# Optimization experiments

Measured on AMD Instinct MI355X. Metric: run time of the kernel, lower is better.

The kernel has to match this reference:

```python
import jax, jax.numpy as jnp
import numpy as np

N = 50000
E = 1600000
IN = 128
HID = 128
OUT = 64
NL = 200000
NEG_SLOPE = 0.2


def _glorot(key, shape):
    fan_in, fan_out = shape[0], shape[-1]
    s = jnp.sqrt(6.0 / (fan_in + fan_out))
    return jax.random.uniform(key, shape, jnp.float32, -s, s)


def setup_inputs() -> dict:
    key = jax.random.key(0)
    ks = jax.random.split(key, 16)
    x = jax.random.normal(ks[0], (N, IN), jnp.float32)
    edge_index = jax.random.randint(ks[1], (2, E), 0, N, dtype=jnp.int32)
    edge_label_index = jax.random.randint(ks[2], (2, NL), 0, N, dtype=jnp.int32)
    return {
        "x": x,
        "edge_index": edge_index,
        "edge_label_index": edge_label_index,
        "W1": _glorot(ks[3], (IN, HID)),  "a1s": _glorot(ks[4], (HID,)),  "a1d": _glorot(ks[5], (HID,)),  "b1": jnp.zeros((HID,), jnp.float32),
        "W2": _glorot(ks[6], (HID, HID)), "a2s": _glorot(ks[7], (HID,)),  "a2d": _glorot(ks[8], (HID,)),  "b2": jnp.zeros((HID,), jnp.float32),
        "W3": _glorot(ks[9], (HID, HID)), "a3s": _glorot(ks[10], (HID,)), "a3d": _glorot(ks[11], (HID,)), "b3": jnp.zeros((HID,), jnp.float32),
        "W4": _glorot(ks[12], (HID, OUT)), "b4": jnp.zeros((OUT,), jnp.float32),
    }


def _add_self_loops(edge_index, n):
    loop = jnp.arange(n, dtype=edge_index.dtype)
    return jnp.concatenate([edge_index, jnp.stack([loop, loop])], axis=1)


def gat_conv(x, edge_index, W, a_s, a_d, b):
    """PyG GATConv, heads=1, add_self_loops=True: gather, LeakyReLU score,
    segment softmax over destination nodes, scatter-add aggregate."""
    n = x.shape[0]
    ei = _add_self_loops(edge_index, n)
    src, dst = ei[0], ei[1]
    h = x @ W                                    # [N, H]
    e = jax.nn.leaky_relu((h @ a_s)[src] + (h @ a_d)[dst], NEG_SLOPE)  # [E']
    m = jax.ops.segment_max(e, dst, num_segments=n)
    p = jnp.exp(e - m[dst])
    s = jax.ops.segment_sum(p, dst, num_segments=n)
    alpha = p / s[dst]                           # segment softmax
    out = jax.ops.segment_sum(h[src] * alpha[:, None], dst, num_segments=n)
    return out + b


def gcn_conv(x, edge_index, W, b):
    """PyG GCNConv: self-loops + symmetric degree normalization."""
    n = x.shape[0]
    ei = _add_self_loops(edge_index, n)
    src, dst = ei[0], ei[1]
    h = x @ W
    deg = jax.ops.segment_sum(jnp.ones(src.shape, h.dtype), dst, num_segments=n)
    dinv = jax.lax.rsqrt(deg)
    norm = dinv[src] * dinv[dst]                 # [E']
    out = jax.ops.segment_sum(h[src] * norm[:, None], dst, num_segments=n)
    return out + b


def reference(x, edge_index, edge_label_index,
              W1, a1s, a1d, b1, W2, a2s, a2d, b2,
              W3, a3s, a3d, b3, W4, b4):
    h = jax.nn.relu(gat_conv(x, edge_index, W1, a1s, a1d, b1))
    h = jax.nn.relu(gat_conv(h, edge_index, W2, a2s, a2d, b2))
    h = jax.nn.relu(gat_conv(h, edge_index, W3, a3s, a3d, b3))
    z = gcn_conv(h, edge_index, W4, b4)          # [N, OUT]
    # decode: dot product of endpoint embeddings -> link logits [NL]
    return (z[edge_label_index[0]] * z[edge_label_index[1]]).sum(axis=-1)
```

## Files before the change

### kernel.cpp

```cpp
#include <hip/hip_runtime.h>
#include <hip/hip_fp16.h>
#include <math.h>

#define NN   50000
#define NE   1600000
#define DHID 128
#define DOUTC 64
#define NLBL 200000
#define CAP  80
#define NEG  0.2f
#define NBK  196
#define CAPB 8800
#define CHK  4096

typedef unsigned short u16;
typedef _Float16 half8 __attribute__((ext_vector_type(8)));
typedef float floatx4 __attribute__((ext_vector_type(4)));
typedef unsigned int u32x4 __attribute__((ext_vector_type(4)));


__global__ __launch_bounds__(256) void k_bin(const int* __restrict__ ei,
                                             int* __restrict__ gcnt,
                                             unsigned* __restrict__ bins) {
    __shared__ int cntL[NBK];
    __shared__ int offL[NBK];
    __shared__ int curL[NBK];
    __shared__ int curG[NBK];
    __shared__ unsigned stage[CHK];
    const int tid = threadIdx.x;
    const int e0 = blockIdx.x * CHK + tid * 16;
    const bool act = (e0 + 15) < NE;

    unsigned pk[16];
    int bb[16];
    if (act) {
#pragma unroll
        for (int g = 0; g < 4; ++g) {
            int4 s4 = *(const int4*)&ei[e0 + g * 4];
            int4 d4 = *(const int4*)&ei[NE + e0 + g * 4];
            int sa[4] = {s4.x, s4.y, s4.z, s4.w};
            int da[4] = {d4.x, d4.y, d4.z, d4.w};
#pragma unroll
            for (int k = 0; k < 4; ++k) {
                int idx = g * 4 + k;
                bb[idx] = da[k] >> 8;
                pk[idx] = (unsigned)sa[k] | ((unsigned)(da[k] & 255) << 16)
                        | ((unsigned)bb[idx] << 24);
            }
        }
    }
    for (int i = tid; i < NBK; i += 256) cntL[i] = 0;
    __syncthreads();
    if (act) {
#pragma unroll
        for (int k = 0; k < 16; ++k) atomicAdd(&cntL[bb[k]], 1);
    }
    __syncthreads();
    if (tid < NBK) {
        int acc = 0;
        for (int i = 0; i < tid; ++i) acc += cntL[i];
        offL[tid] = acc;
        curL[tid] = acc;
    }
    __syncthreads();
    for (int i = tid; i < NBK; i += 256) curG[i] = atomicAdd(&gcnt[i], cntL[i]);
    __syncthreads();
    if (act) {
#pragma unroll
        for (int k = 0; k < 16; ++k) {
            int pos = atomicAdd(&curL[bb[k]], 1);
            stage[pos] = pk[k];
        }
    }
    __syncthreads();
    const int tot = offL[NBK - 1] + cntL[NBK - 1];
    for (int j = tid; j < tot; j += 256) {
        unsigned v = stage[j];
        int b = v >> 24;
        int lr = j - offL[b];
        bins[(size_t)b * CAPB + curG[b] + lr] = v & 0x00FFFFFFu;
    }
}

__global__ __launch_bounds__(256) void k_build(const unsigned* __restrict__ bins,
                                               const int* __restrict__ gcnt,
                                               int* __restrict__ cnt,
                                               u16* __restrict__ csr) {
    __shared__ u16 rows[256 * CAP];
    __shared__ int cur[256];
    const int b = blockIdx.x, tid = threadIdx.x;
    const int d0 = b << 8;
    const int nd = min(256, NN - d0);
    if (tid < nd) { cur[tid] = 1; rows[tid * CAP] = (u16)(d0 + tid); }
    __syncthreads();
    const int n = gcnt[b];
    for (int i = tid; i < n; i += 256) {
        unsigned v = bins[(size_t)b * CAPB + i];
        int s = v & 0xFFFF, dl = (v >> 16) & 0xFF;
        int pos = atomicAdd(&cur[dl], 1);
        if (pos < CAP) rows[dl * CAP + pos] = (u16)s;
    }
    __syncthreads();
    const unsigned* rw = (const unsigned*)rows;
    unsigned* cw = (unsigned*)(csr + (size_t)d0 * CAP);
    const int tot = nd * (CAP / 2);
    for (int i = tid; i < tot; i += 256) cw[i] = rw[i];
    if (tid < nd) cnt[d0 + tid] = cur[tid];
}


__global__ __launch_bounds__(256) void k_prep_w(const float* __restrict__ W1f,
                                                const float* __restrict__ W2f,
                                                const float* __restrict__ W3f,
                                                const float* __restrict__ W4f,
                                                half8* __restrict__ Wf1,
                                                half8* __restrict__ Wf2,
                                                half8* __restrict__ Wf3,
                                                half8* __restrict__ Wf4,
                                                int* __restrict__ gcnt) {
    if (blockIdx.x == 28) {
        int i = threadIdx.x;
        if (i < NBK) gcnt[i] = 0;
        return;
    }
    int e = blockIdx.x * 256 + threadIdx.x;
    const float* W;
    half8* Wf;
    int nout, le;
    if (e < 2048)      { W = W1f; Wf = Wf1; nout = 128; le = e; }
    else if (e < 4096) { W = W2f; Wf = Wf2; nout = 128; le = e - 2048; }
    else if (e < 6144) { W = W3f; Wf = Wf3; nout = 128; le = e - 4096; }
    else               { W = W4f; Wf = Wf4; nout = 64;  le = e - 6144; }
    int c = le >> 8, rem = le & 255, ks = rem >> 6, lane = rem & 63;
    int n = lane & 15, quad = lane >> 4;
    int col = c * 16 + n, k0 = ks * 32 + quad * 8;
    half8 v;
#pragma unroll
    for (int j = 0; j < 8; ++j) v[j] = (_Float16)W[(size_t)(k0 + j) * nout + col];
    Wf[le] = v;
}


template <int NOUT, bool ATTN, typename TA>
__global__ __launch_bounds__(256) void gemm_mfma(const TA* __restrict__ A0,
                                                 const TA* __restrict__ A1,
                                                 const half8* __restrict__ Wf,
                                                 __half* __restrict__ C0,
                                                 __half* __restrict__ C1,
                                                 const float* __restrict__ a_s,
                                                 const float* __restrict__ a_d,
                                                 float* __restrict__ asv,
                                                 float* __restrict__ adv, int M) {
    constexpr int CT = NOUT / 16;
    const int tid = threadIdx.x;
    const int wave = tid >> 6, lane = tid & 63;
    const int n = lane & 15, quad = lane >> 4;
    const int row0 = blockIdx.x * 64 + wave * 16;

    const int row = row0 + n;
    const bool ok = row < M;
    half8 a[4];
    half8 zz = {};
#pragma unroll
    for (int ks = 0; ks < 4; ++ks) {
        if (!ok) { a[ks] = zz; continue; }
        int c128 = ks * 32 + quad * 8;
        if constexpr (sizeof(TA) == 2) {
            const TA* Ah = (c128 < 64) ? A0 : A1;
            a[ks] = *(const half8*)((const _Float16*)Ah + (size_t)row * 64 + (c128 & 63));
        } else {
            const float* Ap = (const float*)A0 + (size_t)row * 128 + c128;
            float4 f0 = *(const float4*)Ap;
            float4 f1 = *(const float4*)(Ap + 4);
            half8 v;
            v[0] = (_Float16)f0.x; v[1] = (_Float16)f0.y; v[2] = (_Float16)f0.z; v[3] = (_Float16)f0.w;
            v[4] = (_Float16)f1.x; v[5] = (_Float16)f1.y; v[6] = (_Float16)f1.z; v[7] = (_Float16)f1.w;
            a[ks] = v;
        }
    }

    floatx4 acc[CT];
#pragma unroll
    for (int c = 0; c < CT; ++c) acc[c] = (floatx4){0.f, 0.f, 0.f, 0.f};

#pragma unroll
    for (int c = 0; c < CT; ++c) {
#pragma unroll
        for (int ks = 0; ks < 4; ++ks) {
            half8 b = Wf[(c * 4 + ks) * 64 + lane];
            acc[c] = __builtin_amdgcn_mfma_f32_16x16x32_f16(b, a[ks], acc[c], 0, 0, 0);
        }
    }

    if (ok) {
#pragma unroll
        for (int c = 0; c < CT; ++c) {
            __half* Ch = (NOUT == 64 || c < 4) ? C0 : C1;
            int coff = (NOUT == 64 || c < 4) ? c * 16 : (c - 4) * 16;
            __half2 h0 = __floats2half2_rn(acc[c][0], acc[c][1]);
            __half2 h1 = __floats2half2_rn(acc[c][2], acc[c][3]);
            uint2 u;
            __builtin_memcpy(&u.x, &h0, 4);
            __builtin_memcpy(&u.y, &h1, 4);
            *(uint2*)&Ch[(size_t)row * 64 + coff + quad * 4] = u;
        }
    }

    if (ATTN) {
        float ps = 0.f, pd = 0.f;
#pragma unroll
        for (int c = 0; c < CT; ++c) {
#pragma unroll
            for (int reg = 0; reg < 4; ++reg) {
                float w = acc[c][reg];
                ps = fmaf(w, a_s[c * 16 + quad * 4 + reg], ps);
                pd = fmaf(w, a_d[c * 16 + quad * 4 + reg], pd);
            }
        }
        ps += __shfl_xor(ps, 16); ps += __shfl_xor(ps, 32);
        pd += __shfl_xor(pd, 16); pd += __shfl_xor(pd, 32);
        if (quad == 0 && ok) { asv[row] = ps; adv[row] = pd; }
    }
}

__device__ inline void fma_h8v(half8 h, float al, float* acc) {
#pragma unroll
    for (int k = 0; k < 8; ++k) acc[k] = fmaf(al, (float)h[k], acc[k]);
}


__global__ __launch_bounds__(256) void k_gat_agg(const __half* __restrict__ h0,
                                                 const __half* __restrict__ h1,
                                                 const int* __restrict__ cnt,
                                                 const u16* __restrict__ csr,
                                                 const float* __restrict__ asv,
                                                 const float* __restrict__ adv,
                                                 const float* __restrict__ bias,
                                                 __half* __restrict__ out0,
                                                 __half* __restrict__ out1) {
    __shared__ float alsL[4][88];
    __shared__ int   srcL[4][88];
    int lane = threadIdx.x & 63, wv = threadIdx.x >> 6;
    int d = blockIdx.x * 4 + wv;
    if (d >= NN) return;
    int deg = cnt[d]; if (deg > CAP) deg = CAP;
    const float advd = adv[d];
    const u16* rowp = csr + (size_t)d * CAP;

    int j0 = lane, j1 = lane + 64;
    int s0 = 0, s1 = 0;
    float e0 = -INFINITY, e1 = -INFINITY;
    if (j0 < deg) {
        s0 = rowp[j0];
        float t = asv[s0] + advd;
        e0 = (t >= 0.f) ? t : NEG * t;
    }
    if (j1 < deg) {
        s1 = rowp[j1];
        float t = asv[s1] + advd;
        e1 = (t >= 0.f) ? t : NEG * t;
    }
    float m = fmaxf(e0, e1);
#pragma unroll
    for (int off = 32; off; off >>= 1) m = fmaxf(m, __shfl_xor(m, off));
    float p0 = (j0 < deg) ? __expf(e0 - m) : 0.f;
    float p1 = (j1 < deg) ? __expf(e1 - m) : 0.f;
    float s = p0 + p1;
#pragma unroll
    for (int off = 32; off; off >>= 1) s += __shfl_xor(s, off);
    float inv = 1.f / s;
    alsL[wv][j0] = p0 * inv;
    srcL[wv][j0] = s0;
    if (j1 < 88) { alsL[wv][j1] = p1 * inv; srcL[wv][j1] = s1; }

    int slot = lane >> 3, r = lane & 7;
    int degp = (deg + 7) & ~7;
#pragma unroll
    for (int half = 0; half < 2; ++half) {
        const __half* ht = half ? h1 : h0;
        __half* ot = half ? out1 : out0;
        float acc[8];
#pragma unroll
        for (int k = 0; k < 8; ++k) acc[k] = 0.f;

        for (int base = 0; base < degp; base += 8) {
            int idx = base + slot;
            float al = alsL[wv][idx];
            int   sj = srcL[wv][idx];
            half8 hv = *(const half8*)&ht[(size_t)sj * 64 + r * 8];
            fma_h8v(hv, al, acc);
        }
#pragma unroll
        for (int k = 0; k < 8; ++k) {
            acc[k] += __shfl_xor(acc[k], 8);
            acc[k] += __shfl_xor(acc[k], 16);
            acc[k] += __shfl_xor(acc[k], 32);
        }
        if (slot == 0) {
            __half2 ho[4];
#pragma unroll
            for (int k = 0; k < 4; ++k) {
                float oa = fmaxf(acc[2 * k]     + bias[half * 64 + r * 8 + 2 * k],     0.f);
                float ob = fmaxf(acc[2 * k + 1] + bias[half * 64 + r * 8 + 2 * k + 1], 0.f);
                ho[k] = __floats2half2_rn(oa, ob);
            }
            u32x4 u;
            __builtin_memcpy(&u, &ho[0], 16);
            __builtin_nontemporal_store(u, (u32x4*)&ot[(size_t)d * 64 + r * 8]);
        }
    }
}


__global__ __launch_bounds__(256) void k_gcn_agg(const __half* __restrict__ h,
                                                 const int* __restrict__ cnt,
                                                 const u16* __restrict__ csr,
                                                 const float* __restrict__ bias,
                                                 __half* __restrict__ z) {
    __shared__ float nmL[4][88];
    __shared__ int   srcL[4][88];
    int lane = threadIdx.x & 63, wv = threadIdx.x >> 6;
    int d = blockIdx.x * 4 + wv;
    if (d >= NN) return;
    int degc = cnt[d];
    int deg = degc > CAP ? CAP : degc;
    float did = rsqrtf((float)degc);
    const u16* rowp = csr + (size_t)d * CAP;

    int j0 = lane, j1 = lane + 64;
    int s0 = 0, s1 = 0;
    float n0 = 0.f, n1 = 0.f;
    if (j0 < deg) { s0 = rowp[j0]; n0 = rsqrtf((float)cnt[s0]) * did; }
    if (j1 < deg) { s1 = rowp[j1]; n1 = rsqrtf((float)cnt[s1]) * did; }
    nmL[wv][j0] = n0;
    srcL[wv][j0] = s0;
    if (j1 < 88) { nmL[wv][j1] = n1; srcL[wv][j1] = s1; }

    int slot = lane >> 3, r = lane & 7;
    float acc[8];
#pragma unroll
    for (int k = 0; k < 8; ++k) acc[k] = 0.f;

    int degp = (deg + 7) & ~7;
    for (int base = 0; base < degp; base += 8) {
        int idx = base + slot;
        float nm = nmL[wv][idx];
        int   sj = srcL[wv][idx];
        half8 hv = *(const half8*)&h[(size_t)sj * 64 + r * 8];
        fma_h8v(hv, nm, acc);
    }
#pragma unroll
    for (int k = 0; k < 8; ++k) {
        acc[k] += __shfl_xor(acc[k], 8);
        acc[k] += __shfl_xor(acc[k], 16);
        acc[k] += __shfl_xor(acc[k], 32);
    }
    if (slot == 0) {
        __half2 ho[4];
#pragma unroll
        for (int k = 0; k < 4; ++k) {
            float oa = acc[2 * k]     + bias[r * 8 + 2 * k];
            float ob = acc[2 * k + 1] + bias[r * 8 + 2 * k + 1];
            ho[k] = __floats2half2_rn(oa, ob);
        }
        uint4 u;
        __builtin_memcpy(&u, &ho[0], 16);
        *(uint4*)&z[(size_t)d * 64 + r * 8] = u;
    }
}


__global__ __launch_bounds__(256) void k_decode(const __half* __restrict__ z,
                                                const int* __restrict__ eli,
                                                float* __restrict__ outp) {
    int lane = threadIdx.x & 63, wv = threadIdx.x >> 6;
    int g = lane >> 4, r = lane & 15;
    int idx = (blockIdx.x * 4 + wv) * 4 + g;
    if (idx >= NLBL) return;
    int a = eli[idx], b = eli[NLBL + idx];
    uint2 ua = *(const uint2*)&z[(size_t)a * 64 + r * 4];
    uint2 ub = *(const uint2*)&z[(size_t)b * 64 + r * 4];
    float2 a0 = __half22float2(*(__half2*)&ua.x);
    float2 a1 = __half22float2(*(__half2*)&ua.y);
    float2 b0 = __half22float2(*(__half2*)&ub.x);
    float2 b1 = __half22float2(*(__half2*)&ub.y);
    float v = a0.x * b0.x + a0.y * b0.y + a1.x * b1.x + a1.y * b1.y;
#pragma unroll
    for (int off = 8; off; off >>= 1) v += __shfl_xor(v, off);
    if (r == 0) outp[idx] = v;
}


extern "C" void kernel_launch(void* const* d_in, const int* in_sizes, int n_in,
                              void* d_out, int out_size, void* d_ws, size_t ws_size,
                              hipStream_t stream) {
    const float* x   = (const float*)d_in[0];
    const int*   ei  = (const int*)d_in[1];
    const int*   eli = (const int*)d_in[2];
    const float* W1 = (const float*)d_in[3];
    const float* a1s = (const float*)d_in[4];
    const float* a1d = (const float*)d_in[5];
    const float* b1 = (const float*)d_in[6];
    const float* W2 = (const float*)d_in[7];
    const float* a2s = (const float*)d_in[8];
    const float* a2d = (const float*)d_in[9];
    const float* b2 = (const float*)d_in[10];
    const float* W3 = (const float*)d_in[11];
    const float* a3s = (const float*)d_in[12];
    const float* a3d = (const float*)d_in[13];
    const float* b3 = (const float*)d_in[14];
    const float* W4 = (const float*)d_in[15];
    const float* b4 = (const float*)d_in[16];
    float* outp = (float*)d_out;

    char* p = (char*)d_ws;
    auto alloc = [&](size_t bytes) -> char* {
        char* r = p;
        p += (bytes + 255) & ~(size_t)255;
        return r;
    };
    int*    cnt  = (int*)alloc((size_t)NN * 4);
    u16*    csr  = (u16*)alloc((size_t)NN * CAP * 2);
    int*    gcnt = (int*)alloc((size_t)NBK * 4);
    float*  asv  = (float*)alloc((size_t)NN * 4);
    float*  advv = (float*)alloc((size_t)NN * 4);
    __half* G0   = (__half*)alloc((size_t)NN * 64 * 2);
    __half* G1   = (__half*)alloc((size_t)NN * 64 * 2);
    __half* B1a  = (__half*)alloc((size_t)NN * 64 * 2);
    __half* B1b  = (__half*)alloc((size_t)NN * 64 * 2);
    __half* B2a  = (__half*)alloc((size_t)NN * 64 * 2);
    __half* B2b  = (__half*)alloc((size_t)NN * 64 * 2);
    __half* zf   = (__half*)alloc((size_t)NN * 64 * 2);
    half8*  Wf1  = (half8*)alloc(2048 * 16);
    half8*  Wf2  = (half8*)alloc(2048 * 16);
    half8*  Wf3  = (half8*)alloc(2048 * 16);
    half8*  Wf4  = (half8*)alloc(1024 * 16);
    unsigned* bins = (unsigned*)alloc((size_t)NBK * CAPB * 4);

    const int gBin  = (NE + CHK - 1) / CHK;
    const int gGemm = (NN + 63) / 64;
    const int gNode = (NN + 3) / 4;
    const int gDec  = (NLBL + 15) / 16;

    k_prep_w<<<29, 256, 0, stream>>>(W1, W2, W3, W4, Wf1, Wf2, Wf3, Wf4, gcnt);
    k_bin<<<gBin, 256, 0, stream>>>(ei, gcnt, bins);
    k_build<<<NBK, 256, 0, stream>>>(bins, gcnt, cnt, csr);

    gemm_mfma<128, true, float><<<gGemm, 256, 0, stream>>>(x, x, Wf1, G0, G1, a1s, a1d, asv, advv, NN);
    k_gat_agg<<<gNode, 256, 0, stream>>>(G0, G1, cnt, csr, asv, advv, b1, B1a, B1b);

    gemm_mfma<128, true, __half><<<gGemm, 256, 0, stream>>>(B1a, B1b, Wf2, G0, G1, a2s, a2d, asv, advv, NN);
    k_gat_agg<<<gNode, 256, 0, stream>>>(G0, G1, cnt, csr, asv, advv, b2, B2a, B2b);

    gemm_mfma<128, true, __half><<<gGemm, 256, 0, stream>>>(B2a, B2b, Wf3, G0, G1, a3s, a3d, asv, advv, NN);
    k_gat_agg<<<gNode, 256, 0, stream>>>(G0, G1, cnt, csr, asv, advv, b3, B1a, B1b);

    gemm_mfma<64, false, __half><<<gGemm, 256, 0, stream>>>(B1a, B1b, Wf4, G0, G0, nullptr, nullptr, nullptr, nullptr, NN);
    k_gcn_agg<<<gNode, 256, 0, stream>>>(G0, cnt, csr, b4, zf);

    k_decode<<<gDec, 256, 0, stream>>>(zf, eli, outp);
}
```

Before: 383.9 us.

## Fuse edge binning with first-layer GEMM and use single-wave GEMM blocks

Merges the edge-binning kernel and the layer-1 projection GEMM into one launch, with block index choosing the role, so the independent GEMM work can run alongside binning and one launch is saved. The later GEMMs are launched as 64-thread blocks, one 16-row tile each, instead of 256-thread blocks. Bounds checks are simplified because NN is a multiple of 16. The shared-memory footprint of the binning phase now applies to the GEMM blocks too, which may limit occupancy.

```diff
diff --git a/kernel.cpp b/kernel.cpp
--- a/kernel.cpp
+++ b/kernel.cpp
@@ -4,14 +4,13 @@
 
 #define NN   50000
 #define NE   1600000
-#define DHID 128
-#define DOUTC 64
 #define NLBL 200000
 #define CAP  80
 #define NEG  0.2f
 #define NBK  196
 #define CAPB 8800
 #define CHK  4096
+#define GBIN 391
 
 typedef unsigned short u16;
 typedef _Float16 half8 __attribute__((ext_vector_type(8)));
@@ -19,16 +18,15 @@
 typedef unsigned int u32x4 __attribute__((ext_vector_type(4)));
 
 
-__global__ __launch_bounds__(256) void k_bin(const int* __restrict__ ei,
-                                             int* __restrict__ gcnt,
-                                             unsigned* __restrict__ bins) {
+__device__ void ph_bin(int blk, const int* __restrict__ ei,
+                       int* __restrict__ gcnt, unsigned* __restrict__ bins) {
     __shared__ int cntL[NBK];
     __shared__ int offL[NBK];
     __shared__ int curL[NBK];
     __shared__ int curG[NBK];
     __shared__ unsigned stage[CHK];
     const int tid = threadIdx.x;
-    const int e0 = blockIdx.x * CHK + tid * 16;
+    const int e0 = blk * CHK + tid * 16;
     const bool act = (e0 + 15) < NE;
 
     unsigned pk[16];
@@ -109,15 +107,15 @@
 }
 
 
-__global__ __launch_bounds__(256) void k_prep_w(const float* __restrict__ W1f,
-                                                const float* __restrict__ W2f,
-                                                const float* __restrict__ W3f,
-                                                const float* __restrict__ W4f,
-                                                half8* __restrict__ Wf1,
-                                                half8* __restrict__ Wf2,
-                                                half8* __restrict__ Wf3,
-                                                half8* __restrict__ Wf4,
-                                                int* __restrict__ gcnt) {
+__global__ __launch_bounds__(256) void k_pre(const float* __restrict__ W1f,
+                                             const float* __restrict__ W2f,
+                                             const float* __restrict__ W3f,
+                                             const float* __restrict__ W4f,
+                                             half8* __restrict__ Wf1,
+                                             half8* __restrict__ Wf2,
+                                             half8* __restrict__ Wf3,
+                                             half8* __restrict__ Wf4,
+                                             int* __restrict__ gcnt) {
     if (blockIdx.x == 28) {
         int i = threadIdx.x;
         if (i < NBK) gcnt[i] = 0;
@@ -142,28 +140,24 @@
 
 
 template <int NOUT, bool ATTN, typename TA>
-__global__ __launch_bounds__(256) void gemm_mfma(const TA* __restrict__ A0,
-                                                 const TA* __restrict__ A1,
-                                                 const half8* __restrict__ Wf,
-                                                 __half* __restrict__ C0,
-                                                 __half* __restrict__ C1,
-                                                 const float* __restrict__ a_s,
-                                                 const float* __restrict__ a_d,
-                                                 float* __restrict__ asv,
-                                                 float* __restrict__ adv, int M) {
+__device__ __forceinline__ void gemm_tile(int gt, int lane,
+                                          const TA* __restrict__ A0,
+                                          const TA* __restrict__ A1,
+                                          const half8* __restrict__ Wf,
+                                          __half* __restrict__ C0,
+                                          __half* __restrict__ C1,
+                                          const float* __restrict__ a_s,
+                                          const float* __restrict__ a_d,
+                                          float* __restrict__ asv,
+                                          float* __restrict__ adv) {
     constexpr int CT = NOUT / 16;
-    const int tid = threadIdx.x;
-    const int wave = tid >> 6, lane = tid & 63;
     const int n = lane & 15, quad = lane >> 4;
-    const int row0 = blockIdx.x * 64 + wave * 16;
-
-    const int row = row0 + n;
-    const bool ok = row < M;
+    if (gt * 16 >= NN) return;
+    const int row = gt * 16 + n;
+
     half8 a[4];
-    half8 zz = {};
 #pragma unroll
     for (int ks = 0; ks < 4; ++ks) {
-        if (!ok) { a[ks] = zz; continue; }
         int c128 = ks * 32 + quad * 8;
         if constexpr (sizeof(TA) == 2) {
             const TA* Ah = (c128 < 64) ? A0 : A1;
@@ -182,7 +176,6 @@
     floatx4 acc[CT];
 #pragma unroll
     for (int c = 0; c < CT; ++c) acc[c] = (floatx4){0.f, 0.f, 0.f, 0.f};
-
 #pragma unroll
     for (int c = 0; c < CT; ++c) {
 #pragma unroll
@@ -192,18 +185,16 @@
         }
     }
 
-    if (ok) {
-#pragma unroll
-        for (int c = 0; c < CT; ++c) {
-            __half* Ch = (NOUT == 64 || c < 4) ? C0 : C1;
-            int coff = (NOUT == 64 || c < 4) ? c * 16 : (c - 4) * 16;
-            __half2 h0 = __floats2half2_rn(acc[c][0], acc[c][1]);
-            __half2 h1 = __floats2half2_rn(acc[c][2], acc[c][3]);
-            uint2 u;
-            __builtin_memcpy(&u.x, &h0, 4);
-            __builtin_memcpy(&u.y, &h1, 4);
-            *(uint2*)&Ch[(size_t)row * 64 + coff + quad * 4] = u;
-        }
+#pragma unroll
+    for (int c = 0; c < CT; ++c) {
+        __half* Ch = (NOUT == 64 || c < 4) ? C0 : C1;
+        int coff = (NOUT == 64 || c < 4) ? c * 16 : (c - 4) * 16;
+        __half2 h0 = __floats2half2_rn(acc[c][0], acc[c][1]);
+        __half2 h1 = __floats2half2_rn(acc[c][2], acc[c][3]);
+        uint2 u;
+        __builtin_memcpy(&u.x, &h0, 4);
+        __builtin_memcpy(&u.y, &h1, 4);
+        *(uint2*)&Ch[(size_t)row * 64 + coff + quad * 4] = u;
     }
 
     if (ATTN) {
@@ -219,11 +210,41 @@
         }
         ps += __shfl_xor(ps, 16); ps += __shfl_xor(ps, 32);
         pd += __shfl_xor(pd, 16); pd += __shfl_xor(pd, 32);
-        if (quad == 0 && ok) { asv[row] = ps; adv[row] = pd; }
-    }
-}
-
-__device__ inline void fma_h8v(half8 h, float al, float* acc) {
+        if (quad == 0) { asv[row] = ps; adv[row] = pd; }
+    }
+}
+
+__global__ __launch_bounds__(256) void k_bin_gemm1(const int* __restrict__ ei,
+                                                   int* __restrict__ gcnt,
+                                                   unsigned* __restrict__ bins,
+                                                   const float* __restrict__ x,
+                                                   const half8* __restrict__ Wf1,
+                                                   __half* __restrict__ G0,
+                                                   __half* __restrict__ G1,
+                                                   const float* __restrict__ a_s,
+                                                   const float* __restrict__ a_d,
+                                                   float* __restrict__ asv,
+                                                   float* __restrict__ adv) {
+    if (blockIdx.x < GBIN) { ph_bin(blockIdx.x, ei, gcnt, bins); return; }
+    int gt = (blockIdx.x - GBIN) * 4 + (threadIdx.x >> 6);
+    gemm_tile<128, true, float>(gt, threadIdx.x & 63, x, x, Wf1, G0, G1, a_s, a_d, asv, adv);
+}
+
+template <int NOUT, bool ATTN>
+__global__ __launch_bounds__(64) void k_gemm64(const __half* __restrict__ A0,
+                                               const __half* __restrict__ A1,
+                                               const half8* __restrict__ Wf,
+                                               __half* __restrict__ C0,
+                                               __half* __restrict__ C1,
+                                               const float* __restrict__ a_s,
+                                               const float* __restrict__ a_d,
+                                               float* __restrict__ asv,
+                                               float* __restrict__ adv) {
+    gemm_tile<NOUT, ATTN, __half>(blockIdx.x, threadIdx.x & 63, A0, A1, Wf, C0, C1,
+                                  a_s, a_d, asv, adv);
+}
+
+__device__ __forceinline__ void fma_h8v(half8 h, float al, float* acc) {
 #pragma unroll
     for (int k = 0; k < 8; ++k) acc[k] = fmaf(al, (float)h[k], acc[k]);
 }
@@ -437,25 +458,24 @@
     half8*  Wf4  = (half8*)alloc(1024 * 16);
     unsigned* bins = (unsigned*)alloc((size_t)NBK * CAPB * 4);
 
-    const int gBin  = (NE + CHK - 1) / CHK;
-    const int gGemm = (NN + 63) / 64;
+    const int gG1   = GBIN + 782;
+    const int gGemm = (NN + 15) / 16;
     const int gNode = (NN + 3) / 4;
     const int gDec  = (NLBL + 15) / 16;
 
-    k_prep_w<<<29, 256, 0, stream>>>(W1, W2, W3, W4, Wf1, Wf2, Wf3, Wf4, gcnt);
-    k_bin<<<gBin, 256, 0, stream>>>(ei, gcnt, bins);
+    k_pre<<<29, 256, 0, stream>>>(W1, W2, W3, W4, Wf1, Wf2, Wf3, Wf4, gcnt);
+    k_bin_gemm1<<<gG1, 256, 0, stream>>>(ei, gcnt, bins, x, Wf1, G0, G1, a1s, a1d, asv, advv);
     k_build<<<NBK, 256, 0, stream>>>(bins, gcnt, cnt, csr);
 
-    gemm_mfma<128, true, float><<<gGemm, 256, 0, stream>>>(x, x, Wf1, G0, G1, a1s, a1d, asv, advv, NN);
     k_gat_agg<<<gNode, 256, 0, stream>>>(G0, G1, cnt, csr, asv, advv, b1, B1a, B1b);
 
-    gemm_mfma<128, true, __half><<<gGemm, 256, 0, stream>>>(B1a, B1b, Wf2, G0, G1, a2s, a2d, asv, advv, NN);
+    k_gemm64<128, true><<<gGemm, 64, 0, stream>>>(B1a, B1b, Wf2, G0, G1, a2s, a2d, asv, advv);
     k_gat_agg<<<gNode, 256, 0, stream>>>(G0, G1, cnt, csr, asv, advv, b2, B2a, B2b);
 
-    gemm_mfma<128, true, __half><<<gGemm, 256, 0, stream>>>(B2a, B2b, Wf3, G0, G1, a3s, a3d, asv, advv, NN);
+    k_gemm64<128, true><<<gGemm, 64, 0, stream>>>(B2a, B2b, Wf3, G0, G1, a3s, a3d, asv, advv);
     k_gat_agg<<<gNode, 256, 0, stream>>>(G0, G1, cnt, csr, asv, advv, b3, B1a, B1b);
 
-    gemm_mfma<64, false, __half><<<gGemm, 256, 0, stream>>>(B1a, B1b, Wf4, G0, G0, nullptr, nullptr, nullptr, nullptr, NN);
+    k_gemm64<64, false><<<gGemm, 64, 0, stream>>>(B1a, B1b, Wf4, G0, G0, nullptr, nullptr, nullptr, nullptr);
     k_gcn_agg<<<gNode, 256, 0, stream>>>(G0, cnt, csr, b4, zf);
 
     k_decode<<<gDec, 256, 0, stream>>>(zf, eli, outp);
```

New measurement: 373.7 us. 1.03x faster.
